# Kernel tuning notes

Hardware: AMD Instinct MI355X
Metric: run time of the kernel (lower is better)

## Reference

```python
import jax, jax.numpy as jnp
import numpy as np

BLOCKS = (1, 2, 3, 4)      # (block_size, offset=0) from max_block_size=4
BLOCK_MULT = 12            # lcm(1,2,3,4)
DS = 4                     # downsample_factor
MAX_BS = 4                 # max block size (also pos_conv kernel size)
DIM = 512
VOCAB = 256


def _masked_mean(t, m, axis):
    # t: [..., L, D], m: [..., L] bool -> mean over axis with mask, 0 where empty
    mf = m[..., None].astype(t.dtype)
    num = jnp.sum(t * mf, axis=axis)
    tot = jnp.sum(mf, axis=axis)
    mean = num / jnp.clip(tot, 1.0)
    return jnp.where(tot == 0.0, jnp.zeros_like(mean), mean)


def setup_inputs() -> dict:
    key = jax.random.key(0)
    ks = jax.random.split(key, 8)
    B, S = 8, 2048
    return {
        "x": jax.random.randint(ks[0], (B, S), 0, VOCAB),
        "mask": jnp.ones((B, S), dtype=bool),
        "emb": jax.random.normal(ks[1], (VOCAB, DIM), jnp.float32) * 0.02,
        "dw_w": jax.random.normal(ks[2], (MAX_BS, 1, DIM), jnp.float32) * 0.1,   # depthwise kernel (W, I=1, O=DIM)
        "dw_b": jnp.zeros((DIM,), jnp.float32),
        "pw_w": jax.random.normal(ks[3], (1, DIM, DIM), jnp.float32) * 0.03,     # pointwise 1x1 conv
        "pw_b": jnp.zeros((DIM,), jnp.float32),
        "score_w": jax.random.normal(ks[4], (DIM, 1), jnp.float32) * 0.05,
        "score_b": jnp.zeros((1,), jnp.float32),
    }


def reference(x, mask, emb, dw_w, dw_b, pw_w, pw_b, score_w, score_b):
    B, S = x.shape
    D = DIM
    trunc = ((S + DS - 1) // DS) * DS  # next_divisible_length(S, DS); equals S here

    h = emb[x]                                              # [B,S,D]
    h = jnp.pad(h, ((0, 0), (0, MAX_BS - 1), (0, 0)))       # right pad for VALID conv
    dn = jax.lax.conv_dimension_numbers(h.shape, dw_w.shape, ('NWC', 'WIO', 'NWC'))
    h = jax.lax.conv_general_dilated(h, dw_w, (1,), 'VALID',
                                     dimension_numbers=dn,
                                     feature_group_count=D) + dw_b  # depthwise -> [B,S,D]
    h = jnp.einsum('bsd,de->bse', h, pw_w[0]) + pw_b                # pointwise

    # pad seq to multiple of lcm of block sizes
    Sp = ((h.shape[1] + BLOCK_MULT - 1) // BLOCK_MULT) * BLOCK_MULT
    pad = Sp - h.shape[1]
    h = jnp.pad(h, ((0, 0), (0, pad), (0, 0)))
    m = jnp.pad(mask.astype(bool), ((0, 0), (0, pad)), constant_values=False)

    reprs, rmasks = [], []
    for bsz in BLOCKS:  # fixed small set of block sizes (offset=0 for all)
        nb = Sp // bsz
        g = h.reshape(B, nb, bsz, D)
        mg = m.reshape(B, nb, bsz)
        r = _masked_mean(g, mg, axis=2)                       # [B,nb,D]
        reprs.append(jnp.repeat(r, bsz, axis=1))              # [B,Sp,D]
        rmasks.append(jnp.repeat(jnp.any(mg, axis=-1), bsz, axis=1))

    block_reprs = jnp.stack(reprs, axis=2)    # [B,Sp,M,D]
    block_masks = jnp.stack(rmasks, axis=2)   # [B,Sp,M]

    scores = (block_reprs @ score_w)[..., 0] + score_b[0]     # [B,Sp,M]
    max_neg = -jnp.finfo(scores.dtype).max
    scores = jnp.where(block_masks, scores, max_neg)
    scores = jnp.nan_to_num(jax.nn.softmax(scores, axis=2), nan=0.0)

    # consensus attention over positions
    sim = jnp.einsum('bim,bjm->bij', scores, scores)          # [B,Sp,Sp]
    cm = m[:, :, None] & m[:, None, :]
    sim = jnp.where(cm, sim, max_neg)
    attn = jnp.nan_to_num(jax.nn.softmax(sim, axis=-1), nan=0.0)
    scores = jnp.einsum('bij,bjm->bim', attn, scores)

    out = jnp.einsum('bsmd,bsm->bsd', block_reprs, scores)    # weighted combine
    out = out[:, :trunc]
    mt = m[:, :trunc]

    nl = trunc // DS
    xb = out.reshape(B, nl, DS, D)
    mb = mt.reshape(B, nl, DS)
    out = _masked_mean(xb, mb, axis=2)                        # [B, S/DS, D]
    out_mask = jnp.any(mb, axis=-1)
    return out, out_mask
```

## Files before the change

kernel.cpp:

```cpp
#include <hip/hip_runtime.h>
#include <stdint.h>
#include <stddef.h>

typedef __bf16 bf16_t;
typedef bf16_t bf16x4v __attribute__((ext_vector_type(4)));
typedef bf16_t bf16x8v __attribute__((ext_vector_type(8)));
typedef float  f32x4   __attribute__((ext_vector_type(4)));

#define NBATCH 8
#define SEQ    2048
#define DIM    512
#define SP     2052
#define NB2    1026
#define NB3    684
#define NB4    513
#define NL     512

static __device__ __forceinline__ f32x4 ldbf4(const bf16_t* p) {
  bf16x4v v = *(const bf16x4v*)p;
  f32x4 r;
  r.x = (float)v[0]; r.y = (float)v[1]; r.z = (float)v[2]; r.w = (float)v[3];
  return r;
}
static __device__ __forceinline__ void stbf4(bf16_t* p, f32x4 v) {
  bf16x4v o;
  o[0] = (bf16_t)v.x; o[1] = (bf16_t)v.y; o[2] = (bf16_t)v.z; o[3] = (bf16_t)v.w;
  *(bf16x4v*)p = o;
}

static __device__ __forceinline__ void gload_lds16(const void* g, void* l) {
  __builtin_amdgcn_global_load_lds(
      (const __attribute__((address_space(1))) void*)g,
      (__attribute__((address_space(3))) void*)l, 16, 0, 0);
}

#define GA_WT   256
#define GA_MASK 65
#define GA_A    (NBATCH * SEQ / 2)
__global__ __launch_bounds__(256) void kA_prep(
    const float* __restrict__ pw, bf16_t* __restrict__ Wt,
    const void* __restrict__ mraw, float* __restrict__ mask01,
    const int* __restrict__ x, const float* __restrict__ emb,
    const float* __restrict__ dww, const float* __restrict__ dwb,
    bf16_t* __restrict__ A) {
  const int bx = blockIdx.x, t = threadIdx.x;
  if (bx < GA_WT) {
    __shared__ float T[32][33];
    int ti = bx >> 4, tj = bx & 15;
    int r = t >> 3, c0 = (t & 7) * 4;
    f32x4 v = *(const f32x4*)(pw + (size_t)(ti * 32 + r) * DIM + tj * 32 + c0);
    T[c0 + 0][r] = v.x; T[c0 + 1][r] = v.y;
    T[c0 + 2][r] = v.z; T[c0 + 3][r] = v.w;
    __syncthreads();
    bf16x4v o;
    o[0] = (bf16_t)T[r][c0 + 0]; o[1] = (bf16_t)T[r][c0 + 1];
    o[2] = (bf16_t)T[r][c0 + 2]; o[3] = (bf16_t)T[r][c0 + 3];
    *(bf16x4v*)(Wt + (size_t)(tj * 32 + r) * DIM + ti * 32 + c0) = o;
    return;
  }
  if (bx < GA_WT + GA_MASK) {
    int idx = (bx - GA_WT) * 256 + t;
    if (idx >= NBATCH * SP) return;
    int b = idx / SP, s = idx - b * SP;
    const unsigned char* mb = (const unsigned char*)mraw;
    int u8 = 0;
#pragma unroll
    for (int i = 0; i < 64; i++)
      if ((i & 3) != 0 && mb[i] != 0) u8 = 1;
    float v = 0.f;
    if (s < SEQ) {
      int mi = b * SEQ + s;
      int nz = u8 ? (mb[mi] != 0) : (((const int*)mraw)[mi] != 0);
      v = nz ? 1.f : 0.f;
    }
    mask01[idx] = v;
    return;
  }
  int rp = bx - (GA_WT + GA_MASK);
  int row = rp * 2 + (t >> 7);
  int b = row >> 11, s = row & 2047;
  int d0 = (t & 127) * 4;
  f32x4 acc = *(const f32x4*)(dwb + d0);
#pragma unroll
  for (int tt = 0; tt < 4; tt++) {
    int sp = s + tt;
    if (sp < SEQ) {
      int v = x[b * SEQ + sp];
      f32x4 e = *(const f32x4*)(emb + (size_t)v * DIM + d0);
      f32x4 w = *(const f32x4*)(dww + tt * DIM + d0);
      acc += e * w;
    }
  }
  stbf4(A + (size_t)row * DIM + d0, acc);
}

#define BM 64
#define BN 128
#define BK 32
__global__ __launch_bounds__(256) void k2_gemm(
    const bf16_t* __restrict__ A, const bf16_t* __restrict__ Bt,
    const float* __restrict__ bias, bf16_t* __restrict__ H) {
  __shared__ __align__(16) bf16_t As[BM * BK];
  __shared__ __align__(16) bf16_t Bs[BN * BK];
  const int t = threadIdx.x;
  const int bid = blockIdx.x;
  const int xcd = bid & 7, loc = bid >> 3;
  const int mt = xcd * 32 + (loc >> 2);
  const int nt = loc & 3;
  const int m0 = mt * BM, n0 = nt * BN;
  const int lane = t & 63, wave = t >> 6;
  const int wm = (wave & 1) * 32, wn = (wave >> 1) * 64;
  const int mloc = lane & 15, quad = lane >> 4;

  f32x4 acc[2][4] = {};

  char* asd  = (char*)As + t * 16;
  char* bsd1 = (char*)Bs + t * 16;
  char* bsd2 = (char*)Bs + (t + 256) * 16;
  const int ar = t >> 2, ak = (t & 3) * 8;
  const int br2 = (t + 256) >> 2;

  for (int k0 = 0; k0 < 512; k0 += BK) {
    gload_lds16(A + (size_t)(m0 + ar) * DIM + k0 + ak, asd);
    gload_lds16(Bt + (size_t)(n0 + ar) * DIM + k0 + ak, bsd1);
    gload_lds16(Bt + (size_t)(n0 + br2) * DIM + k0 + ak, bsd2);
    __syncthreads();
    bf16x8v af[2], bfr[4];
#pragma unroll
    for (int i = 0; i < 2; i++)
      af[i] = *(const bf16x8v*)&As[(wm + i * 16 + mloc) * BK + quad * 8];
#pragma unroll
    for (int i = 0; i < 4; i++)
      bfr[i] = *(const bf16x8v*)&Bs[(wn + i * 16 + mloc) * BK + quad * 8];
#pragma unroll
    for (int mi = 0; mi < 2; mi++)
#pragma unroll
      for (int ni = 0; ni < 4; ni++)
        acc[mi][ni] = __builtin_amdgcn_mfma_f32_16x16x32_bf16(
            af[mi], bfr[ni], acc[mi][ni], 0, 0, 0);
    __syncthreads();
  }
#pragma unroll
  for (int ni = 0; ni < 4; ni++) {
    int col = n0 + wn + ni * 16 + mloc;
    float bv = bias[col];
#pragma unroll
    for (int mi = 0; mi < 2; mi++) {
      int rbase = m0 + wm + mi * 16 + quad * 4;
#pragma unroll
      for (int r = 0; r < 4; r++)
        H[(size_t)(rbase + r) * DIM + col] = (bf16_t)(acc[mi][ni][r] + bv);
    }
  }
}

__global__ __launch_bounds__(128) void kB_levels(
    const bf16_t* __restrict__ H, const float* __restrict__ mask01,
    const float* __restrict__ sw, const float* __restrict__ sbp,
    bf16_t* __restrict__ R2, bf16_t* __restrict__ R3, bf16_t* __restrict__ R4,
    float* __restrict__ P) {
  const int b = blockIdx.x, c = blockIdx.y;
  const int s0 = c * 12;
  const int t = threadIdx.x;
  const int d0 = t * 4;
  const float sb = sbp[0];

  f32x4 h[12];
  float ms[12], p[12];
  f32x4 swv = *(const f32x4*)(sw + d0);
#pragma unroll
  for (int i = 0; i < 12; i++) {
    int s = s0 + i;
    ms[i] = mask01[b * SP + s];
    if (s < SEQ) {
      h[i] = ldbf4(H + ((size_t)b * SEQ + s) * DIM + d0);
    } else {
      h[i].x = h[i].y = h[i].z = h[i].w = 0.f;
    }
    p[i] = h[i].x * swv.x + h[i].y * swv.y + h[i].z * swv.z + h[i].w * swv.w;
  }
#pragma unroll
  for (int j = 0; j < 6; j++) {
    int i0 = 2 * j;
    float cc = ms[i0] + ms[i0 + 1];
    f32x4 sm = h[i0] * ms[i0] + h[i0 + 1] * ms[i0 + 1];
    float sc = cc > 0.f ? 1.f / cc : 0.f;
    stbf4(R2 + ((size_t)b * NB2 + (c * 6 + j)) * DIM + d0, sm * sc);
  }
#pragma unroll
  for (int j = 0; j < 4; j++) {
    int i0 = 3 * j;
    float cc = ms[i0] + ms[i0 + 1] + ms[i0 + 2];
    f32x4 sm = h[i0] * ms[i0] + h[i0 + 1] * ms[i0 + 1] + h[i0 + 2] * ms[i0 + 2];
    float sc = cc > 0.f ? 1.f / cc : 0.f;
    stbf4(R3 + ((size_t)b * NB3 + (c * 4 + j)) * DIM + d0, sm * sc);
  }
#pragma unroll
  for (int j = 0; j < 3; j++) {
    int i0 = 4 * j;
    float cc = ms[i0] + ms[i0 + 1] + ms[i0 + 2] + ms[i0 + 3];
    f32x4 sm = h[i0] * ms[i0] + h[i0 + 1] * ms[i0 + 1] +
               h[i0 + 2] * ms[i0 + 2] + h[i0 + 3] * ms[i0 + 3];
    float sc = cc > 0.f ? 1.f / cc : 0.f;
    stbf4(R4 + ((size_t)b * NB4 + (c * 3 + j)) * DIM + d0, sm * sc);
  }
#pragma unroll
  for (int off = 32; off > 0; off >>= 1)
#pragma unroll
    for (int i = 0; i < 12; i++) p[i] += __shfl_down(p[i], off);
  __shared__ float hsw[2][12];
  int lane = t & 63, wv = t >> 6;
  if (lane == 0)
#pragma unroll
    for (int i = 0; i < 12; i++) hsw[wv][i] = p[i];
  __syncthreads();
#define HSUM(i) (hsw[0][i] + hsw[1][i])
  if (t < 12) {
    int i = t;
    float m1 = ms[i];
    float v1 = HSUM(i) * m1 + sb;
    int i2 = i & ~1;
    float cc2 = ms[i2] + ms[i2 + 1];
    float s2 = HSUM(i2) * ms[i2] + HSUM(i2 + 1) * ms[i2 + 1];
    float v2 = (cc2 > 0.f ? s2 / cc2 : 0.f) + sb;
    int i3 = (i >= 9) ? 9 : (i >= 6) ? 6 : (i >= 3) ? 3 : 0;
    float cc3 = ms[i3] + ms[i3 + 1] + ms[i3 + 2];
    float s3 = HSUM(i3) * ms[i3] + HSUM(i3 + 1) * ms[i3 + 1] +
               HSUM(i3 + 2) * ms[i3 + 2];
    float v3 = (cc3 > 0.f ? s3 / cc3 : 0.f) + sb;
    int i4 = i & ~3;
    float cc4 = ms[i4] + ms[i4 + 1] + ms[i4 + 2] + ms[i4 + 3];
    float s4 = HSUM(i4) * ms[i4] + HSUM(i4 + 1) * ms[i4 + 1] +
               HSUM(i4 + 2) * ms[i4 + 2] + HSUM(i4 + 3) * ms[i4 + 3];
    float v4 = (cc4 > 0.f ? s4 / cc4 : 0.f) + sb;
    const float NEG = -3.0e38f;
    float a1 = m1 > 0.f ? v1 : NEG, a2 = cc2 > 0.f ? v2 : NEG;
    float a3 = cc3 > 0.f ? v3 : NEG, a4 = cc4 > 0.f ? v4 : NEG;
    float mx = fmaxf(fmaxf(a1, a2), fmaxf(a3, a4));
    f32x4 o;
    if (mx <= NEG) {
      o.x = o.y = o.z = o.w = 0.25f;
    } else {
      float e1 = m1 > 0.f ? __expf(v1 - mx) : 0.f;
      float e2 = cc2 > 0.f ? __expf(v2 - mx) : 0.f;
      float e3 = cc3 > 0.f ? __expf(v3 - mx) : 0.f;
      float e4 = cc4 > 0.f ? __expf(v4 - mx) : 0.f;
      float inv = 1.f / (e1 + e2 + e3 + e4);
      o.x = e1 * inv; o.y = e2 * inv; o.z = e3 * inv; o.w = e4 * inv;
    }
    *(f32x4*)(P + ((size_t)b * SP + s0 + i) * 4) = o;
  }
#undef HSUM
}

__global__ __launch_bounds__(256) void k56_attn_out(
    const float* __restrict__ P, const float* __restrict__ mask01,
    const bf16_t* __restrict__ H, const bf16_t* __restrict__ R2,
    const bf16_t* __restrict__ R3, const bf16_t* __restrict__ R4,
    float* __restrict__ out, float* __restrict__ omask) {
  __shared__ float Px[SP], Py[SP], Pz[SP], Pw[SP];
  __shared__ f32x4 ws4[32];
  __shared__ float msk[32];
  __shared__ float c4w[4];
  const int b = blockIdx.x, lbase = blockIdx.y * 8;
  const int t = threadIdx.x;
  const int w = t >> 6, lane = t & 63;

  float cnt0 = 0.f;
  for (int j = t; j < SP; j += 256) {
    f32x4 q = *(const f32x4*)(P + ((size_t)b * SP + j) * 4);
    float mf = mask01[b * SP + j];
    if (mf == 0.f) {
      q.x = q.y = q.z = q.w = 0.f;
      cnt0 += 1.f;
    }
    Px[j] = q.x; Py[j] = q.y; Pz[j] = q.z; Pw[j] = q.w;
  }
#pragma unroll
  for (int off = 32; off > 0; off >>= 1) cnt0 += __shfl_down(cnt0, off);
  if (lane == 0) c4w[w] = cnt0;
  __syncthreads();
  const float nmv = c4w[0] + c4w[1] + c4w[2] + c4w[3];

#pragma unroll 1
  for (int k = 0; k < 8; k++) {
    int sl = w * 8 + k;
    int s = lbase * 4 + sl;
    float qx = Px[s], qy = Py[s], qz = Pz[s], qw = Pw[s];
    float ax = 0.f, ay = 0.f, az = 0.f, aw = 0.f, den = 0.f;
    for (int j = lane; j < SP; j += 64) {
      float px = Px[j], py = Py[j], pz = Pz[j], pw4 = Pw[j];
      float e = __expf(qx * px + qy * py + qz * pz + qw * pw4);
      den += e;
      ax += e * px; ay += e * py; az += e * pz; aw += e * pw4;
    }
#pragma unroll
    for (int off = 32; off > 0; off >>= 1) {
      ax += __shfl_down(ax, off); ay += __shfl_down(ay, off);
      az += __shfl_down(az, off); aw += __shfl_down(aw, off);
      den += __shfl_down(den, off);
    }
    if (lane == 0) {
      den -= nmv;
      float inv = den > 0.f ? 1.f / den : 0.f;
      f32x4 wv4; wv4.x = ax * inv; wv4.y = ay * inv;
      wv4.z = az * inv; wv4.w = aw * inv;
      ws4[sl] = wv4;
      msk[sl] = mask01[b * SP + s];
    }
  }
  __syncthreads();

#pragma unroll 1
  for (int p = 0; p < 4; p++) {
    int ll = p * 2 + (t >> 7);
    int l = lbase + ll;
    int d0 = (t & 127) * 4;
    f32x4 o; o.x = o.y = o.z = o.w = 0.f;
    float cnt = 0.f;
#pragma unroll
    for (int si = 0; si < 4; si++) {
      int sl = ll * 4 + si;
      int s = l * 4 + si;
      float m = msk[sl];
      f32x4 wv4 = ws4[sl];
      f32x4 r1 = ldbf4(H + ((size_t)b * SEQ + s) * DIM + d0);
      f32x4 r2 = ldbf4(R2 + ((size_t)b * NB2 + (s >> 1)) * DIM + d0);
      f32x4 r3 = ldbf4(R3 + ((size_t)b * NB3 + (s / 3)) * DIM + d0);
      f32x4 r4 = ldbf4(R4 + ((size_t)b * NB4 + (s >> 2)) * DIM + d0);
      o += m * (wv4.x * r1 + wv4.y * r2 + wv4.z * r3 + wv4.w * r4);
      cnt += m;
    }
    float inv = cnt > 0.f ? 1.f / cnt : 0.f;
    o *= inv;
    *(f32x4*)(out + ((size_t)b * NL + l) * DIM + d0) = o;
    if ((t & 127) == 0) omask[b * NL + l] = cnt > 0.f ? 1.f : 0.f;
  }
}

extern "C" void kernel_launch(void* const* d_in, const int* in_sizes, int n_in,
                              void* d_out, int out_size, void* d_ws, size_t ws_size,
                              hipStream_t stream) {
  const int*   x    = (const int*)d_in[0];
  const void*  mraw = d_in[1];
  const float* emb  = (const float*)d_in[2];
  const float* dww  = (const float*)d_in[3];
  const float* dwb  = (const float*)d_in[4];
  const float* pw   = (const float*)d_in[5];
  const float* pwb  = (const float*)d_in[6];
  const float* sw   = (const float*)d_in[7];
  const float* sb   = (const float*)d_in[8];

  char* ws = (char*)d_ws;
  size_t off = 0;
  auto alloc = [&](size_t bytes) {
    size_t o = off;
    off = (off + bytes + 255) & ~(size_t)255;
    return o;
  };
  bf16_t* A    = (bf16_t*)(ws + alloc((size_t)NBATCH * SEQ * DIM * 2));
  bf16_t* H    = (bf16_t*)(ws + alloc((size_t)NBATCH * SEQ * DIM * 2));
  bf16_t* Wt   = (bf16_t*)(ws + alloc((size_t)DIM * DIM * 2));
  bf16_t* R2   = (bf16_t*)(ws + alloc((size_t)NBATCH * NB2 * DIM * 2));
  bf16_t* R3   = (bf16_t*)(ws + alloc((size_t)NBATCH * NB3 * DIM * 2));
  bf16_t* R4   = (bf16_t*)(ws + alloc((size_t)NBATCH * NB4 * DIM * 2));
  float* mask01 = (float*)(ws + alloc((size_t)NBATCH * SP * 4));
  float* P     = (float*)(ws + alloc((size_t)NBATCH * SP * 4 * 4));

  float* out   = (float*)d_out;
  float* omask = out + (size_t)NBATCH * NL * DIM;

  kA_prep<<<GA_WT + GA_MASK + GA_A, 256, 0, stream>>>(pw, Wt, mraw, mask01,
                                                      x, emb, dww, dwb, A);
  k2_gemm<<<1024, 256, 0, stream>>>(A, Wt, pwb, H);
  kB_levels<<<dim3(NBATCH, 171), 128, 0, stream>>>(H, mask01, sw, sb,
                                                   R2, R3, R4, P);
  k56_attn_out<<<dim3(NBATCH, 64), 256, 0, stream>>>(P, mask01, H, R2, R3, R4,
                                                     out, omask);
}
```

Before: 153.1 us.

## Precompute vocab-by-tap GEMM table instead of per-token embedding conv GEMM

Exploits linearity: embedding, depthwise conv and pointwise projection are folded into a 1024-row table G (256 vocab entries × 4 taps), each row being emb*dw_w projected through pw, plus a folded bias. The 16K-row GEMM shrinks to a 1K-row GEMM, and H is rebuilt on the fly in the level and output kernels by summing four gathered G rows per position. This removes the large A and H intermediates and most of the GEMM work, at the cost of four gathers per position in two kernels and some bf16 rounding differences.

```diff
diff --git a/kernel.cpp b/kernel.cpp
--- a/kernel.cpp
+++ b/kernel.cpp
@@ -34,17 +34,18 @@
       (__attribute__((address_space(3))) void*)l, 16, 0, 0);
 }
 
-#define GA_WT   256
-#define GA_MASK 65
-#define GA_A    (NBATCH * SEQ / 2)
-__global__ __launch_bounds__(256) void kA_prep(
+#define GP_WT   256
+#define GP_MASK 65
+#define GP_AP   512
+#define GP_B2   2
+__global__ __launch_bounds__(256) void kPrep(
     const float* __restrict__ pw, bf16_t* __restrict__ Wt,
     const void* __restrict__ mraw, float* __restrict__ mask01,
-    const int* __restrict__ x, const float* __restrict__ emb,
-    const float* __restrict__ dww, const float* __restrict__ dwb,
-    bf16_t* __restrict__ A) {
+    const float* __restrict__ emb, const float* __restrict__ dww,
+    const float* __restrict__ dwb, const float* __restrict__ pwb,
+    bf16_t* __restrict__ Ap, float* __restrict__ bias2) {
   const int bx = blockIdx.x, t = threadIdx.x;
-  if (bx < GA_WT) {
+  if (bx < GP_WT) {
     __shared__ float T[32][33];
     int ti = bx >> 4, tj = bx & 15;
     int r = t >> 3, c0 = (t & 7) * 4;
@@ -58,8 +59,8 @@
     *(bf16x4v*)(Wt + (size_t)(tj * 32 + r) * DIM + ti * 32 + c0) = o;
     return;
   }
-  if (bx < GA_WT + GA_MASK) {
-    int idx = (bx - GA_WT) * 256 + t;
+  if (bx < GP_WT + GP_MASK) {
+    int idx = (bx - GP_WT) * 256 + t;
     if (idx >= NBATCH * SP) return;
     int b = idx / SP, s = idx - b * SP;
     const unsigned char* mb = (const unsigned char*)mraw;
@@ -76,37 +77,35 @@
     mask01[idx] = v;
     return;
   }
-  int rp = bx - (GA_WT + GA_MASK);
-  int row = rp * 2 + (t >> 7);
-  int b = row >> 11, s = row & 2047;
-  int d0 = (t & 127) * 4;
-  f32x4 acc = *(const f32x4*)(dwb + d0);
-#pragma unroll
-  for (int tt = 0; tt < 4; tt++) {
-    int sp = s + tt;
-    if (sp < SEQ) {
-      int v = x[b * SEQ + sp];
-      f32x4 e = *(const f32x4*)(emb + (size_t)v * DIM + d0);
-      f32x4 w = *(const f32x4*)(dww + tt * DIM + d0);
-      acc += e * w;
-    }
-  }
-  stbf4(A + (size_t)row * DIM + d0, acc);
+  if (bx < GP_WT + GP_MASK + GP_AP) {
+    int rp = bx - (GP_WT + GP_MASK);
+    int row = rp * 2 + (t >> 7);
+    int v = row & 255, tt = row >> 8;
+    int d0 = (t & 127) * 4;
+    f32x4 e = *(const f32x4*)(emb + (size_t)v * DIM + d0);
+    f32x4 w = *(const f32x4*)(dww + tt * DIM + d0);
+    stbf4(Ap + (size_t)row * DIM + d0, e * w);
+    return;
+  }
+  {
+    int e = (bx - (GP_WT + GP_MASK + GP_AP)) * 256 + t;
+    float acc = pwb[e];
+#pragma unroll 8
+    for (int d = 0; d < DIM; d++) acc += dwb[d] * pw[(size_t)d * DIM + e];
+    bias2[e] = acc;
+  }
 }
 
 #define BM 64
 #define BN 128
 #define BK 32
-__global__ __launch_bounds__(256) void k2_gemm(
+__global__ __launch_bounds__(256) void kG_gemm(
     const bf16_t* __restrict__ A, const bf16_t* __restrict__ Bt,
-    const float* __restrict__ bias, bf16_t* __restrict__ H) {
+    bf16_t* __restrict__ G) {
   __shared__ __align__(16) bf16_t As[BM * BK];
   __shared__ __align__(16) bf16_t Bs[BN * BK];
   const int t = threadIdx.x;
-  const int bid = blockIdx.x;
-  const int xcd = bid & 7, loc = bid >> 3;
-  const int mt = xcd * 32 + (loc >> 2);
-  const int nt = loc & 3;
+  const int mt = blockIdx.x >> 2, nt = blockIdx.x & 3;
   const int m0 = mt * BM, n0 = nt * BN;
   const int lane = t & 63, wave = t >> 6;
   const int wm = (wave & 1) * 32, wn = (wave >> 1) * 64;
@@ -143,19 +142,19 @@
 #pragma unroll
   for (int ni = 0; ni < 4; ni++) {
     int col = n0 + wn + ni * 16 + mloc;
-    float bv = bias[col];
 #pragma unroll
     for (int mi = 0; mi < 2; mi++) {
       int rbase = m0 + wm + mi * 16 + quad * 4;
 #pragma unroll
       for (int r = 0; r < 4; r++)
-        H[(size_t)(rbase + r) * DIM + col] = (bf16_t)(acc[mi][ni][r] + bv);
-    }
-  }
-}
-
-__global__ __launch_bounds__(128) void kB_levels(
-    const bf16_t* __restrict__ H, const float* __restrict__ mask01,
+        G[(size_t)(rbase + r) * DIM + col] = (bf16_t)acc[mi][ni][r];
+    }
+  }
+}
+
+__global__ __launch_bounds__(128) void kBH_levels(
+    const int* __restrict__ x, const bf16_t* __restrict__ G,
+    const float* __restrict__ bias2, const float* __restrict__ mask01,
     const float* __restrict__ sw, const float* __restrict__ sbp,
     bf16_t* __restrict__ R2, bf16_t* __restrict__ R3, bf16_t* __restrict__ R4,
     float* __restrict__ P) {
@@ -164,7 +163,14 @@
   const int t = threadIdx.x;
   const int d0 = t * 4;
   const float sb = sbp[0];
-
+  __shared__ int xs[15];
+  if (t < 15) {
+    int sidx = s0 + t;
+    xs[t] = (sidx < SEQ) ? x[b * SEQ + sidx] : -1;
+  }
+  __syncthreads();
+
+  f32x4 b2 = *(const f32x4*)(bias2 + d0);
   f32x4 h[12];
   float ms[12], p[12];
   f32x4 swv = *(const f32x4*)(sw + d0);
@@ -173,7 +179,14 @@
     int s = s0 + i;
     ms[i] = mask01[b * SP + s];
     if (s < SEQ) {
-      h[i] = ldbf4(H + ((size_t)b * SEQ + s) * DIM + d0);
+      f32x4 acc = b2;
+#pragma unroll
+      for (int tt = 0; tt < 4; tt++) {
+        int xv = xs[i + tt];
+        if (xv >= 0)
+          acc += ldbf4(G + (size_t)(xv + 256 * tt) * DIM + d0);
+      }
+      h[i] = acc;
     } else {
       h[i].x = h[i].y = h[i].z = h[i].w = 0.f;
     }
@@ -255,17 +268,24 @@
 
 __global__ __launch_bounds__(256) void k56_attn_out(
     const float* __restrict__ P, const float* __restrict__ mask01,
-    const bf16_t* __restrict__ H, const bf16_t* __restrict__ R2,
+    const int* __restrict__ x, const bf16_t* __restrict__ G,
+    const float* __restrict__ bias2, const bf16_t* __restrict__ R2,
     const bf16_t* __restrict__ R3, const bf16_t* __restrict__ R4,
     float* __restrict__ out, float* __restrict__ omask) {
   __shared__ float Px[SP], Py[SP], Pz[SP], Pw[SP];
   __shared__ f32x4 ws4[32];
   __shared__ float msk[32];
   __shared__ float c4w[4];
+  __shared__ int xs[35];
   const int b = blockIdx.x, lbase = blockIdx.y * 8;
   const int t = threadIdx.x;
   const int w = t >> 6, lane = t & 63;
-
+  const int smin = lbase * 4;
+
+  if (t < 35) {
+    int sidx = smin + t;
+    xs[t] = (sidx < SEQ) ? x[b * SEQ + sidx] : -1;
+  }
   float cnt0 = 0.f;
   for (int j = t; j < SP; j += 256) {
     f32x4 q = *(const f32x4*)(P + ((size_t)b * SP + j) * 4);
@@ -285,7 +305,7 @@
 #pragma unroll 1
   for (int k = 0; k < 8; k++) {
     int sl = w * 8 + k;
-    int s = lbase * 4 + sl;
+    int s = smin + sl;
     float qx = Px[s], qy = Py[s], qz = Pz[s], qw = Pw[s];
     float ax = 0.f, ay = 0.f, az = 0.f, aw = 0.f, den = 0.f;
     for (int j = lane; j < SP; j += 64) {
@@ -311,11 +331,12 @@
   }
   __syncthreads();
 
+  const int d0 = (t & 127) * 4;
+  const f32x4 b2 = *(const f32x4*)(bias2 + d0);
 #pragma unroll 1
   for (int p = 0; p < 4; p++) {
     int ll = p * 2 + (t >> 7);
     int l = lbase + ll;
-    int d0 = (t & 127) * 4;
     f32x4 o; o.x = o.y = o.z = o.w = 0.f;
     float cnt = 0.f;
 #pragma unroll
@@ -324,7 +345,13 @@
       int s = l * 4 + si;
       float m = msk[sl];
       f32x4 wv4 = ws4[sl];
-      f32x4 r1 = ldbf4(H + ((size_t)b * SEQ + s) * DIM + d0);
+      f32x4 r1 = b2;
+#pragma unroll
+      for (int tt = 0; tt < 4; tt++) {
+        int xv = xs[sl + tt];
+        if (xv >= 0)
+          r1 += ldbf4(G + (size_t)(xv + 256 * tt) * DIM + d0);
+      }
       f32x4 r2 = ldbf4(R2 + ((size_t)b * NB2 + (s >> 1)) * DIM + d0);
       f32x4 r3 = ldbf4(R3 + ((size_t)b * NB3 + (s / 3)) * DIM + d0);
       f32x4 r4 = ldbf4(R4 + ((size_t)b * NB4 + (s >> 2)) * DIM + d0);
@@ -358,9 +385,10 @@
     off = (off + bytes + 255) & ~(size_t)255;
     return o;
   };
-  bf16_t* A    = (bf16_t*)(ws + alloc((size_t)NBATCH * SEQ * DIM * 2));
-  bf16_t* H    = (bf16_t*)(ws + alloc((size_t)NBATCH * SEQ * DIM * 2));
+  bf16_t* Ap   = (bf16_t*)(ws + alloc((size_t)1024 * DIM * 2));
+  bf16_t* G    = (bf16_t*)(ws + alloc((size_t)1024 * DIM * 2));
   bf16_t* Wt   = (bf16_t*)(ws + alloc((size_t)DIM * DIM * 2));
+  float* bias2 = (float*)(ws + alloc((size_t)DIM * 4));
   bf16_t* R2   = (bf16_t*)(ws + alloc((size_t)NBATCH * NB2 * DIM * 2));
   bf16_t* R3   = (bf16_t*)(ws + alloc((size_t)NBATCH * NB3 * DIM * 2));
   bf16_t* R4   = (bf16_t*)(ws + alloc((size_t)NBATCH * NB4 * DIM * 2));
@@ -370,11 +398,11 @@
   float* out   = (float*)d_out;
   float* omask = out + (size_t)NBATCH * NL * DIM;
 
-  kA_prep<<<GA_WT + GA_MASK + GA_A, 256, 0, stream>>>(pw, Wt, mraw, mask01,
-                                                      x, emb, dww, dwb, A);
-  k2_gemm<<<1024, 256, 0, stream>>>(A, Wt, pwb, H);
-  kB_levels<<<dim3(NBATCH, 171), 128, 0, stream>>>(H, mask01, sw, sb,
-                                                   R2, R3, R4, P);
-  k56_attn_out<<<dim3(NBATCH, 64), 256, 0, stream>>>(P, mask01, H, R2, R3, R4,
-                                                     out, omask);
-}
+  kPrep<<<GP_WT + GP_MASK + GP_AP + GP_B2, 256, 0, stream>>>(
+      pw, Wt, mraw, mask01, emb, dww, dwb, pwb, Ap, bias2);
+  kG_gemm<<<64, 256, 0, stream>>>(Ap, Wt, G);
+  kBH_levels<<<dim3(NBATCH, 171), 128, 0, stream>>>(x, G, bias2, mask01,
+                                                    sw, sb, R2, R3, R4, P);
+  k56_attn_out<<<dim3(NBATCH, 64), 256, 0, stream>>>(P, mask01, x, G, bias2,
+                                                     R2, R3, R4, out, omask);
+}
```

After: 174.1 us. +13.7%, slower.
